# Kernel tuning notes

Hardware: AMD Instinct MI355X
Metric: run time of the kernel (lower is better)

The kernel has to match this reference:

```python
import jax, jax.numpy as jnp
import numpy as np

N_NODES = 50000
N_EDGES = 800000
IN_CH, HID_CH, OUT_CH = 128, 128, 64


def _glorot(key, out_c, in_c):
    lim = (6.0 / (in_c + out_c)) ** 0.5
    return jax.random.uniform(key, (out_c, in_c), jnp.float32, -lim, lim)


def setup_inputs() -> dict:
    key = jax.random.key(0)
    ks = jax.random.split(key, 12)
    x = jax.random.normal(ks[0], (N_NODES, IN_CH), jnp.float32)
    edge_index = jax.random.randint(ks[1], (2, N_EDGES), 0, N_NODES, dtype=jnp.int64)
    # 4 SAGEConv layers: 128->128, 128->128, 128->64, 64->64
    dims = [(IN_CH, HID_CH), (HID_CH, HID_CH), (HID_CH, OUT_CH), (OUT_CH, OUT_CH)]
    params = {}
    for i, (ci, co) in enumerate(dims, start=1):
        params[f"Wl{i}"] = _glorot(ks[2 * i], co, ci)          # neighbor (aggregated) transform
        params[f"bl{i}"] = jnp.zeros((co,), jnp.float32)
        params[f"Wr{i}"] = _glorot(ks[2 * i + 1], co, ci)      # root/self transform (no bias in PyG)
    return {"x": x, "edge_index": edge_index, **params}


def _sage_conv(x, src, dst, Wl, bl, Wr):
    # mean aggregation of source features at destination nodes
    msgs = x[src]                                                   # [E, C] gather
    summed = jax.ops.segment_sum(msgs, dst, num_segments=N_NODES)   # [N, C] scatter-add
    cnt = jax.ops.segment_sum(jnp.ones((src.shape[0], 1), x.dtype), dst, num_segments=N_NODES)
    mean = summed / jnp.maximum(cnt, 1.0)
    return mean @ Wl.T + bl + x @ Wr.T


def reference(x, edge_index, Wl1, bl1, Wr1, Wl2, bl2, Wr2, Wl3, bl3, Wr3, Wl4, bl4, Wr4):
    src, dst = edge_index[0], edge_index[1]
    # conv1 = GraphSAGE(in, hid, num_layers=2): relu between layers only
    h = jax.nn.relu(_sage_conv(x, src, dst, Wl1, bl1, Wr1))
    h = _sage_conv(h, src, dst, Wl2, bl2, Wr2)
    h = jax.nn.relu(h)  # model-level .relu()
    # conv2 = GraphSAGE(hid, out, num_layers=2)
    h = jax.nn.relu(_sage_conv(h, src, dst, Wl3, bl3, Wr3))
    h = _sage_conv(h, src, dst, Wl4, bl4, Wr4)
    return jax.nn.log_softmax(h, axis=1)
```

## Files before the change

### kernel.cpp

```cpp
#include <hip/hip_runtime.h>
#include <hip/hip_bf16.h>


typedef __attribute__((ext_vector_type(8))) short bf16x8;
typedef __attribute__((ext_vector_type(4))) float f32x4;

#define NBKT 512
#define BSHIFT 7
#define BCAP 3072
#define EPB 2048

__device__ __forceinline__ unsigned short f2bf(float f) {
    __hip_bfloat16 h = __float2bfloat16(f);
    return __builtin_bit_cast(unsigned short, h);
}
__device__ __forceinline__ float bflo(unsigned int u) {
    return __builtin_bit_cast(float, u << 16);
}
__device__ __forceinline__ float bfhi(unsigned int u) {
    return __builtin_bit_cast(float, u & 0xffff0000u);
}

__global__ __launch_bounds__(256) void wconv(
    const float* __restrict__ s0, const float* __restrict__ s1,
    const float* __restrict__ s2, const float* __restrict__ s3,
    const float* __restrict__ s4, const float* __restrict__ s5,
    const float* __restrict__ s6, const float* __restrict__ s7,
    unsigned short* __restrict__ wb, int* __restrict__ gcur)
{
    const int b = blockIdx.x;
    if (b == 0) {
        for (int i = threadIdx.x; i < NBKT; i += 256) gcur[i] = 0;
    }
    const float* src;
    int seg_blk, dst_off;
    if      (b < 16) { src = s0; seg_blk = b;      dst_off = 0; }
    else if (b < 32) { src = s1; seg_blk = b - 16; dst_off = 16384; }
    else if (b < 48) { src = s2; seg_blk = b - 32; dst_off = 32768; }
    else if (b < 64) { src = s3; seg_blk = b - 48; dst_off = 49152; }
    else if (b < 72) { src = s4; seg_blk = b - 64; dst_off = 65536; }
    else if (b < 80) { src = s5; seg_blk = b - 72; dst_off = 73728; }
    else if (b < 84) { src = s6; seg_blk = b - 80; dst_off = 81920; }
    else             { src = s7; seg_blk = b - 84; dst_off = 86016; }
    int i = seg_blk * 1024 + threadIdx.x * 4;
    float4 v = *reinterpret_cast<const float4*>(src + i);
    ushort4 o = {f2bf(v.x), f2bf(v.y), f2bf(v.z), f2bf(v.w)};
    *reinterpret_cast<ushort4*>(wb + dst_off + i) = o;
}

__global__ __launch_bounds__(256) void partition_edges(
    const int* __restrict__ ei, int E,
    int* __restrict__ gcur, unsigned int* __restrict__ ppk)
{
    __shared__ int hist[NBKT];
    __shared__ int base[NBKT];
    const int tid = threadIdx.x;
    for (int i = tid; i < NBKT; i += 256) hist[i] = 0;
    __syncthreads();

    const int e0 = blockIdx.x * EPB;
    int bket[8], rank[8];
    unsigned int pk[8];
    #pragma unroll
    for (int k = 0; k < 8; ++k) {
        int e = e0 + k * 256 + tid;
        bket[k] = -1;
        if (e < E) {
            int d = ei[E + e], s = ei[e];
            int b = d >> BSHIFT;
            bket[k] = b;
            pk[k] = ((unsigned int)(d & ((1 << BSHIFT) - 1)) << 16) | (unsigned int)s;
            rank[k] = atomicAdd(&hist[b], 1);
        }
    }
    __syncthreads();
    for (int i = tid; i < NBKT; i += 256)
        base[i] = hist[i] ? atomicAdd(&gcur[i], hist[i]) : 0;
    __syncthreads();
    #pragma unroll
    for (int k = 0; k < 8; ++k) {
        if (bket[k] >= 0) {
            int off = base[bket[k]] + rank[k];
            if (off < BCAP)
                ppk[(size_t)bket[k] * BCAP + off] = pk[k];
        }
    }
}

__global__ __launch_bounds__(256) void bucket_sort(
    const unsigned int* __restrict__ ppk, const int* __restrict__ gcur,
    int* __restrict__ offs, int* __restrict__ srcs, int N, int E)
{
    const int b = blockIdx.x;
    const int tid = threadIdx.x;
    const int lane = tid & 63, wv = tid >> 6;

    int below = 0;
    for (int i = tid; i < NBKT; i += 256) {
        int g = min(gcur[i], BCAP);
        if (i < b) below += g;
    }
    #pragma unroll
    for (int off = 32; off; off >>= 1) below += __shfl_xor(below, off);
    __shared__ int redB[4];
    if (lane == 0) redB[wv] = below;
    __syncthreads();
    const int bb = redB[0] + redB[1] + redB[2] + redB[3];

    const int n = min(gcur[b], BCAP);

    __shared__ unsigned int eL[BCAP];
    __shared__ int cnt[1 << BSHIFT], excl[1 << BSHIFT], cur[1 << BSHIFT];

    if (tid < (1 << BSHIFT)) cnt[tid] = 0;
    for (int i = tid; i < n; i += 256) eL[i] = ppk[(size_t)b * BCAP + i];
    __syncthreads();
    for (int i = tid; i < n; i += 256) atomicAdd(&cnt[eL[i] >> 16], 1);
    __syncthreads();

    int v = 0, x = 0;
    if (tid < 128) {
        v = cnt[tid];
        x = v;
        #pragma unroll
        for (int d = 1; d < 64; d <<= 1) {
            int t = __shfl_up(x, d);
            if ((tid & 63) >= d) x += t;
        }
    }
    __shared__ int w0;
    if (tid == 63) w0 = x;
    __syncthreads();
    if (tid < 128) {
        int incl = x + ((tid >= 64) ? w0 : 0);
        excl[tid] = incl - v;
        cur[tid] = incl - v;
    }
    __syncthreads();

    for (int i = tid; i < n; i += 256) {
        unsigned int pk = eL[i];
        int d = (int)(pk >> 16);
        int pos = atomicAdd(&cur[d], 1);
        srcs[bb + pos] = (int)(pk & 0xffffu);
    }
    if (tid < 128) {
        int gn = (b << BSHIFT) + tid;
        if (gn < N) offs[gn] = bb + excl[tid];
    }
    if (b == gridDim.x - 1 && tid == 0) offs[N] = E;
}

template <int CIN, int COUT, int ZOUTF, int F32IN>
__global__ __launch_bounds__(256) void gemm_all(
    const void* __restrict__ Hv,
    const unsigned short* __restrict__ Wlb, const unsigned short* __restrict__ Wrb,
    unsigned short* __restrict__ Y, unsigned short* __restrict__ Zb,
    float* __restrict__ Zf, int N)
{
    constexpr int BM = 64;
    constexpr int ROWH = CIN + 8;
    __shared__ unsigned short Hs[BM * ROWH];

    const int tid = threadIdx.x;
    const int bm = blockIdx.x * BM;

    if (F32IN) {
        const float* H = (const float*)Hv;
        constexpr int C4 = CIN / 4;
        #pragma unroll
        for (int c = tid; c < BM * C4; c += 256) {
            int row = c / C4, k4 = (c % C4) * 4;
            int g = bm + row;
            float4 v = make_float4(0.f, 0.f, 0.f, 0.f);
            if (g < N) v = *reinterpret_cast<const float4*>(&H[(size_t)g * CIN + k4]);
            ushort4 o = {f2bf(v.x), f2bf(v.y), f2bf(v.z), f2bf(v.w)};
            *reinterpret_cast<ushort4*>(&Hs[row * ROWH + k4]) = o;
        }
    } else {
        const unsigned short* H = (const unsigned short*)Hv;
        constexpr int C8 = CIN / 8;
        #pragma unroll
        for (int c = tid; c < BM * C8; c += 256) {
            int row = c / C8, k8 = (c % C8) * 8;
            int g = bm + row;
            int4 v = {0, 0, 0, 0};
            if (g < N) v = *reinterpret_cast<const int4*>(&H[(size_t)g * CIN + k8]);
            *reinterpret_cast<int4*>(&Hs[row * ROWH + k8]) = v;
        }
    }
    __syncthreads();

    constexpr int TOTC = 2 * COUT;
    constexpr int WCOLS = TOTC / 64;
    constexpr int WROWS = 4 / WCOLS;
    constexpr int MF = BM / (16 * WROWS);
    constexpr int RSPAN = BM / WROWS;

    const int wid = tid >> 6, lane = tid & 63;
    const int wr = wid / WCOLS, wc = wid % WCOLS;
    const int l15 = lane & 15, lhi = lane >> 4;

    f32x4 acc[MF][4] = {};
    #pragma unroll
    for (int k0 = 0; k0 < CIN; k0 += 32) {
        const int colOff = k0 + lhi * 8;
        bf16x8 a[MF], bfr[4];
        #pragma unroll
        for (int m = 0; m < MF; ++m)
            a[m] = *reinterpret_cast<const bf16x8*>(&Hs[(wr * RSPAN + m * 16 + l15) * ROWH + colOff]);
        #pragma unroll
        for (int nn = 0; nn < 4; ++nn) {
            int gcol = wc * 64 + nn * 16 + l15;
            const unsigned short* ws = (gcol < COUT) ? (Wlb + (size_t)gcol * CIN)
                                                     : (Wrb + (size_t)(gcol - COUT) * CIN);
            bfr[nn] = *reinterpret_cast<const bf16x8*>(ws + colOff);
        }
        #pragma unroll
        for (int m = 0; m < MF; ++m)
            #pragma unroll
            for (int nn = 0; nn < 4; ++nn)
                acc[m][nn] = __builtin_amdgcn_mfma_f32_16x16x32_bf16(a[m], bfr[nn], acc[m][nn], 0, 0, 0);
    }

    #pragma unroll
    for (int m = 0; m < MF; ++m) {
        #pragma unroll
        for (int nn = 0; nn < 4; ++nn) {
            int gcol = wc * 64 + nn * 16 + l15;
            #pragma unroll
            for (int j = 0; j < 4; ++j) {
                int grow = bm + wr * RSPAN + m * 16 + lhi * 4 + j;
                if (grow < N) {
                    if (gcol < COUT)      Y[(size_t)grow * COUT + gcol] = f2bf(acc[m][nn][j]);
                    else if (ZOUTF)       Zf[(size_t)grow * COUT + (gcol - COUT)] = acc[m][nn][j];
                    else                  Zb[(size_t)grow * COUT + (gcol - COUT)] = f2bf(acc[m][nn][j]);
                }
            }
        }
    }
}

__global__ __launch_bounds__(256) void agg128_bf(
    const unsigned short* __restrict__ Y, const unsigned short* __restrict__ Zb,
    const float* __restrict__ bl,
    const int* __restrict__ offs, const int* __restrict__ srcs,
    unsigned short* __restrict__ OUT, int N)
{
    const int node = blockIdx.x * 4 + (threadIdx.x >> 6);
    if (node >= N) return;
    const int lane = threadIdx.x & 63;
    const int h = lane >> 5, l31 = lane & 31;
    const int beg = offs[node], end = offs[node + 1];

    float a0 = 0.f, a1 = 0.f, a2 = 0.f, a3 = 0.f;
    int e = beg + h;
    for (; e + 14 < end; e += 16) {
        int s[8];
        #pragma unroll
        for (int j = 0; j < 8; ++j) s[j] = srcs[e + 2 * j];
        uint2 u[8];
        #pragma unroll
        for (int j = 0; j < 8; ++j)
            u[j] = *reinterpret_cast<const uint2*>(&Y[(size_t)s[j] * 128 + 4 * l31]);
        #pragma unroll
        for (int j = 0; j < 8; ++j) {
            a0 += bflo(u[j].x); a1 += bfhi(u[j].x);
            a2 += bflo(u[j].y); a3 += bfhi(u[j].y);
        }
    }
    for (; e + 6 < end; e += 8) {
        int s0 = srcs[e], s1 = srcs[e + 2], s2 = srcs[e + 4], s3 = srcs[e + 6];
        uint2 u0 = *reinterpret_cast<const uint2*>(&Y[(size_t)s0 * 128 + 4 * l31]);
        uint2 u1 = *reinterpret_cast<const uint2*>(&Y[(size_t)s1 * 128 + 4 * l31]);
        uint2 u2 = *reinterpret_cast<const uint2*>(&Y[(size_t)s2 * 128 + 4 * l31]);
        uint2 u3 = *reinterpret_cast<const uint2*>(&Y[(size_t)s3 * 128 + 4 * l31]);
        a0 += bflo(u0.x) + bflo(u1.x) + bflo(u2.x) + bflo(u3.x);
        a1 += bfhi(u0.x) + bfhi(u1.x) + bfhi(u2.x) + bfhi(u3.x);
        a2 += bflo(u0.y) + bflo(u1.y) + bflo(u2.y) + bflo(u3.y);
        a3 += bfhi(u0.y) + bfhi(u1.y) + bfhi(u2.y) + bfhi(u3.y);
    }
    for (; e < end; e += 2) {
        uint2 u = *reinterpret_cast<const uint2*>(&Y[(size_t)srcs[e] * 128 + 4 * l31]);
        a0 += bflo(u.x); a1 += bfhi(u.x); a2 += bflo(u.y); a3 += bfhi(u.y);
    }
    a0 += __shfl_xor(a0, 32);
    a1 += __shfl_xor(a1, 32);
    a2 += __shfl_xor(a2, 32);
    a3 += __shfl_xor(a3, 32);

    if (h == 0) {
        float inv = 1.0f / fmaxf((float)(end - beg), 1.0f);
        uint2 zu = *reinterpret_cast<const uint2*>(&Zb[(size_t)node * 128 + 4 * l31]);
        float4 bb = *reinterpret_cast<const float4*>(&bl[4 * l31]);
        float o0 = fmaxf(a0 * inv + bflo(zu.x) + bb.x, 0.f);
        float o1 = fmaxf(a1 * inv + bfhi(zu.x) + bb.y, 0.f);
        float o2 = fmaxf(a2 * inv + bflo(zu.y) + bb.z, 0.f);
        float o3 = fmaxf(a3 * inv + bfhi(zu.y) + bb.w, 0.f);
        uint2 pk;
        pk.x = (unsigned int)f2bf(o0) | ((unsigned int)f2bf(o1) << 16);
        pk.y = (unsigned int)f2bf(o2) | ((unsigned int)f2bf(o3) << 16);
        *reinterpret_cast<uint2*>(&OUT[(size_t)node * 128 + 4 * l31]) = pk;
    }
}

__global__ __launch_bounds__(256) void agg64_mid(
    const unsigned short* __restrict__ Y, const unsigned short* __restrict__ Zb,
    const float* __restrict__ bl,
    const int* __restrict__ offs, const int* __restrict__ srcs,
    unsigned short* __restrict__ OUT, int N)
{
    const int node = blockIdx.x * 4 + (threadIdx.x >> 6);
    if (node >= N) return;
    const int lane = threadIdx.x & 63;
    const int q = lane >> 4, l15 = lane & 15;
    const int beg = offs[node], end = offs[node + 1];

    float a0 = 0.f, a1 = 0.f, a2 = 0.f, a3 = 0.f;
    int e = beg + q;
    for (; e + 12 < end; e += 16) {
        int s0 = srcs[e], s1 = srcs[e + 4], s2 = srcs[e + 8], s3 = srcs[e + 12];
        uint2 u0 = *reinterpret_cast<const uint2*>(&Y[(size_t)s0 * 64 + 4 * l15]);
        uint2 u1 = *reinterpret_cast<const uint2*>(&Y[(size_t)s1 * 64 + 4 * l15]);
        uint2 u2 = *reinterpret_cast<const uint2*>(&Y[(size_t)s2 * 64 + 4 * l15]);
        uint2 u3 = *reinterpret_cast<const uint2*>(&Y[(size_t)s3 * 64 + 4 * l15]);
        a0 += bflo(u0.x) + bflo(u1.x) + bflo(u2.x) + bflo(u3.x);
        a1 += bfhi(u0.x) + bfhi(u1.x) + bfhi(u2.x) + bfhi(u3.x);
        a2 += bflo(u0.y) + bflo(u1.y) + bflo(u2.y) + bflo(u3.y);
        a3 += bfhi(u0.y) + bfhi(u1.y) + bfhi(u2.y) + bfhi(u3.y);
    }
    for (; e < end; e += 4) {
        uint2 u = *reinterpret_cast<const uint2*>(&Y[(size_t)srcs[e] * 64 + 4 * l15]);
        a0 += bflo(u.x); a1 += bfhi(u.x); a2 += bflo(u.y); a3 += bfhi(u.y);
    }
    a0 += __shfl_xor(a0, 16); a0 += __shfl_xor(a0, 32);
    a1 += __shfl_xor(a1, 16); a1 += __shfl_xor(a1, 32);
    a2 += __shfl_xor(a2, 16); a2 += __shfl_xor(a2, 32);
    a3 += __shfl_xor(a3, 16); a3 += __shfl_xor(a3, 32);

    if (q == 0) {
        float inv = 1.0f / fmaxf((float)(end - beg), 1.0f);
        uint2 zu = *reinterpret_cast<const uint2*>(&Zb[(size_t)node * 64 + 4 * l15]);
        float4 bb = *reinterpret_cast<const float4*>(&bl[4 * l15]);
        float o0 = fmaxf(a0 * inv + bflo(zu.x) + bb.x, 0.f);
        float o1 = fmaxf(a1 * inv + bfhi(zu.x) + bb.y, 0.f);
        float o2 = fmaxf(a2 * inv + bflo(zu.y) + bb.z, 0.f);
        float o3 = fmaxf(a3 * inv + bfhi(zu.y) + bb.w, 0.f);
        uint2 pk;
        pk.x = (unsigned int)f2bf(o0) | ((unsigned int)f2bf(o1) << 16);
        pk.y = (unsigned int)f2bf(o2) | ((unsigned int)f2bf(o3) << 16);
        *reinterpret_cast<uint2*>(&OUT[(size_t)node * 64 + 4 * l15]) = pk;
    }
}

__global__ __launch_bounds__(256) void agg64_lsm(
    const unsigned short* __restrict__ Y, const float* __restrict__ Zf,
    const float* __restrict__ bl,
    const int* __restrict__ offs, const int* __restrict__ srcs,
    float* __restrict__ OUT, int N)
{
    const int node = blockIdx.x * 4 + (threadIdx.x >> 6);
    if (node >= N) return;
    const int lane = threadIdx.x & 63;
    const int q = lane >> 4, l15 = lane & 15;
    const int beg = offs[node], end = offs[node + 1];

    float a0 = 0.f, a1 = 0.f, a2 = 0.f, a3 = 0.f;
    int e = beg + q;
    for (; e + 12 < end; e += 16) {
        int s0 = srcs[e], s1 = srcs[e + 4], s2 = srcs[e + 8], s3 = srcs[e + 12];
        uint2 u0 = *reinterpret_cast<const uint2*>(&Y[(size_t)s0 * 64 + 4 * l15]);
        uint2 u1 = *reinterpret_cast<const uint2*>(&Y[(size_t)s1 * 64 + 4 * l15]);
        uint2 u2 = *reinterpret_cast<const uint2*>(&Y[(size_t)s2 * 64 + 4 * l15]);
        uint2 u3 = *reinterpret_cast<const uint2*>(&Y[(size_t)s3 * 64 + 4 * l15]);
        a0 += bflo(u0.x) + bflo(u1.x) + bflo(u2.x) + bflo(u3.x);
        a1 += bfhi(u0.x) + bfhi(u1.x) + bfhi(u2.x) + bfhi(u3.x);
        a2 += bflo(u0.y) + bflo(u1.y) + bflo(u2.y) + bflo(u3.y);
        a3 += bfhi(u0.y) + bfhi(u1.y) + bfhi(u2.y) + bfhi(u3.y);
    }
    for (; e < end; e += 4) {
        uint2 u = *reinterpret_cast<const uint2*>(&Y[(size_t)srcs[e] * 64 + 4 * l15]);
        a0 += bflo(u.x); a1 += bfhi(u.x); a2 += bflo(u.y); a3 += bfhi(u.y);
    }
    a0 += __shfl_xor(a0, 16); a0 += __shfl_xor(a0, 32);
    a1 += __shfl_xor(a1, 16); a1 += __shfl_xor(a1, 32);
    a2 += __shfl_xor(a2, 16); a2 += __shfl_xor(a2, 32);
    a3 += __shfl_xor(a3, 16); a3 += __shfl_xor(a3, 32);

    float inv = 1.0f / fmaxf((float)(end - beg), 1.0f);
    float4 z = *reinterpret_cast<const float4*>(&Zf[(size_t)node * 64 + 4 * l15]);
    float4 bb = *reinterpret_cast<const float4*>(&bl[4 * l15]);
    float o0 = a0 * inv + z.x + bb.x;
    float o1 = a1 * inv + z.y + bb.y;
    float o2 = a2 * inv + z.z + bb.z;
    float o3 = a3 * inv + z.w + bb.w;

    float m = fmaxf(fmaxf(o0, o1), fmaxf(o2, o3));
    #pragma unroll
    for (int off = 1; off < 16; off <<= 1) m = fmaxf(m, __shfl_xor(m, off));
    float s = expf(o0 - m) + expf(o1 - m) + expf(o2 - m) + expf(o3 - m);
    #pragma unroll
    for (int off = 1; off < 16; off <<= 1) s += __shfl_xor(s, off);
    float ls = logf(s);
    if (q == 0)
        *reinterpret_cast<float4*>(&OUT[(size_t)node * 64 + 4 * l15]) =
            make_float4(o0 - m - ls, o1 - m - ls, o2 - m - ls, o3 - m - ls);
}

extern "C" void kernel_launch(void* const* d_in, const int* in_sizes, int n_in,
                              void* d_out, int out_size, void* d_ws, size_t ws_size,
                              hipStream_t stream) {
    const float* x   = (const float*)d_in[0];
    const int*   ei  = (const int*)d_in[1];
    const float* Wl1 = (const float*)d_in[2];
    const float* bl1 = (const float*)d_in[3];
    const float* Wr1 = (const float*)d_in[4];
    const float* Wl2 = (const float*)d_in[5];
    const float* bl2 = (const float*)d_in[6];
    const float* Wr2 = (const float*)d_in[7];
    const float* Wl3 = (const float*)d_in[8];
    const float* bl3 = (const float*)d_in[9];
    const float* Wr3 = (const float*)d_in[10];
    const float* Wl4 = (const float*)d_in[11];
    const float* bl4 = (const float*)d_in[12];
    const float* Wr4 = (const float*)d_in[13];

    const int N = in_sizes[0] / 128;
    const int E = in_sizes[1] / 2;

    char* p = (char*)d_ws;
    auto alloc = [&](size_t bytes) {
        char* r = p;
        p += (bytes + 255) & ~(size_t)255;
        return r;
    };
    int*            offs  = (int*)alloc((size_t)(N + 1) * 4);
    int*            gcur  = (int*)alloc(NBKT * 4);
    unsigned int*   ppk   = (unsigned int*)alloc((size_t)NBKT * BCAP * 4);
    int*            srcs  = (int*)alloc((size_t)E * 4);
    unsigned short* wb    = (unsigned short*)alloc(90112 * 2);
    unsigned short* yA    = (unsigned short*)alloc((size_t)N * 128 * 2);
    unsigned short* zA    = (unsigned short*)alloc((size_t)N * 128 * 2);
    unsigned short* h1    = (unsigned short*)alloc((size_t)N * 128 * 2);
    unsigned short* h2    = (unsigned short*)alloc((size_t)N * 128 * 2);
    unsigned short* h3    = (unsigned short*)alloc((size_t)N * 64 * 2);
    unsigned short* y3    = (unsigned short*)alloc((size_t)N * 64 * 2);
    unsigned short* z3    = (unsigned short*)alloc((size_t)N * 64 * 2);
    float*          zf4   = (float*)alloc((size_t)N * 64 * 4);
    (void)ws_size; (void)n_in; (void)out_size;

    unsigned short* Wl1b = wb;           unsigned short* Wr1b = wb + 16384;
    unsigned short* Wl2b = wb + 32768;   unsigned short* Wr2b = wb + 49152;
    unsigned short* Wl3b = wb + 65536;   unsigned short* Wr3b = wb + 73728;
    unsigned short* Wl4b = wb + 81920;   unsigned short* Wr4b = wb + 86016;

    const int mtiles = (N + 63) / 64;
    const int nbkt_used = (N + (1 << BSHIFT) - 1) >> BSHIFT;
    const int aggblocks = (N + 3) / 4;

    wconv<<<88, 256, 0, stream>>>(Wl1, Wr1, Wl2, Wr2, Wl3, Wr3, Wl4, Wr4, wb, gcur);

    partition_edges<<<(E + EPB - 1) / EPB, 256, 0, stream>>>(ei, E, gcur, ppk);
    bucket_sort<<<nbkt_used, 256, 0, stream>>>(ppk, gcur, offs, srcs, N, E);

    gemm_all<128, 128, 0, 1><<<mtiles, 256, 0, stream>>>(x, Wl1b, Wr1b, yA, zA, nullptr, N);
    agg128_bf<<<aggblocks, 256, 0, stream>>>(yA, zA, bl1, offs, srcs, h1, N);
    gemm_all<128, 128, 0, 0><<<mtiles, 256, 0, stream>>>(h1, Wl2b, Wr2b, yA, zA, nullptr, N);
    agg128_bf<<<aggblocks, 256, 0, stream>>>(yA, zA, bl2, offs, srcs, h2, N);
    gemm_all<128, 64, 0, 0><<<mtiles, 256, 0, stream>>>(h2, Wl3b, Wr3b, y3, z3, nullptr, N);
    agg64_mid<<<aggblocks, 256, 0, stream>>>(y3, z3, bl3, offs, srcs, h3, N);
    gemm_all<64, 64, 1, 0><<<mtiles, 256, 0, stream>>>(h3, Wl4b, Wr4b, y3, nullptr, zf4, N);
    agg64_lsm<<<aggblocks, 256, 0, stream>>>(y3, zf4, bl4, offs, srcs, (float*)d_out, N);
}
```

Before: 312.5 us.

## Replace atomic bucket scatter with in-LDS bitonic sort for CSR build

Each bucket block now pads its packed (dst,src) edge list to 4096 entries in shared memory and bitonic-sorts it, then writes sources out in sorted order. This replaces the per-destination atomic cursor scatter. The aim is deterministic, coalesced source writes and neighbor lists ordered by source index, which may improve gather locality in the later aggregation passes. The cost is many more barriers and compare-exchange passes in the build kernel, plus a larger LDS footprint.

```diff
diff --git a/kernel.cpp b/kernel.cpp
--- a/kernel.cpp
+++ b/kernel.cpp
@@ -109,13 +109,28 @@
 
     const int n = min(gcur[b], BCAP);
 
-    __shared__ unsigned int eL[BCAP];
-    __shared__ int cnt[1 << BSHIFT], excl[1 << BSHIFT], cur[1 << BSHIFT];
+    __shared__ unsigned int eL[4096];
+    __shared__ int cnt[1 << BSHIFT], excl[1 << BSHIFT];
 
     if (tid < (1 << BSHIFT)) cnt[tid] = 0;
-    for (int i = tid; i < n; i += 256) eL[i] = ppk[(size_t)b * BCAP + i];
+    for (int i = tid; i < 4096; i += 256)
+        eL[i] = (i < n) ? ppk[(size_t)b * BCAP + i] : 0xFFFFFFFFu;
     __syncthreads();
     for (int i = tid; i < n; i += 256) atomicAdd(&cnt[eL[i] >> 16], 1);
+
+    for (unsigned k = 2; k <= 4096; k <<= 1) {
+        for (unsigned j = k >> 1; j > 0; j >>= 1) {
+            __syncthreads();
+            for (int i = tid; i < 4096; i += 256) {
+                int l = i ^ (int)j;
+                if (l > i) {
+                    unsigned a = eL[i], c = eL[l];
+                    bool asc = ((i & (int)k) == 0);
+                    if ((a > c) == asc) { eL[i] = c; eL[l] = a; }
+                }
+            }
+        }
+    }
     __syncthreads();
 
     int v = 0, x = 0;
@@ -131,19 +146,11 @@
     __shared__ int w0;
     if (tid == 63) w0 = x;
     __syncthreads();
-    if (tid < 128) {
-        int incl = x + ((tid >= 64) ? w0 : 0);
-        excl[tid] = incl - v;
-        cur[tid] = incl - v;
-    }
-    __syncthreads();
-
-    for (int i = tid; i < n; i += 256) {
-        unsigned int pk = eL[i];
-        int d = (int)(pk >> 16);
-        int pos = atomicAdd(&cur[d], 1);
-        srcs[bb + pos] = (int)(pk & 0xffffu);
-    }
+    if (tid < 128) excl[tid] = x + ((tid >= 64) ? w0 : 0) - v;
+    __syncthreads();
+
+    for (int i = tid; i < n; i += 256)
+        srcs[bb + i] = (int)(eL[i] & 0xffffu);
     if (tid < 128) {
         int gn = (b << BSHIFT) + tid;
         if (gn < N) offs[gn] = bb + excl[tid];
```

Result: slower. 441.1 us (+41.1%).
